# Performance work log

Measured on AMD Instinct MI355X. Metric: run time of the kernel, lower is better.

## Reference

```python
import jax, jax.numpy as jnp
import numpy as np

N = 8192
E = 262144
H = 64


def setup_inputs() -> dict:
    key = jax.random.key(0)
    ks = jax.random.split(key, 9)
    edge_index = jax.random.randint(ks[0], (2, E), 0, N, dtype=jnp.int64)
    edge_attr = jax.random.uniform(ks[1], (E,), dtype=jnp.float32)
    node_features = jax.random.normal(ks[2], (N, N), dtype=jnp.float32)
    # GCNConv weights (glorot-ish scale) and biases
    W1 = jax.random.normal(ks[3], (N, H), dtype=jnp.float32) / np.sqrt(N)
    b1 = jnp.zeros((H,), dtype=jnp.float32)
    W2 = jax.random.normal(ks[4], (H, H), dtype=jnp.float32) / np.sqrt(H)
    b2 = jnp.zeros((H,), dtype=jnp.float32)
    fcW = jax.random.normal(ks[5], (H, N), dtype=jnp.float32) / np.sqrt(H)
    fcb = jnp.zeros((N,), dtype=jnp.float32)
    return {"edge_index": edge_index, "edge_attr": edge_attr,
            "node_features": node_features,
            "W1": W1, "b1": b1, "W2": W2, "b2": b2,
            "fcW": fcW, "fcb": fcb}


def _gcn_conv(x, W, b, src, dst, ew, n_nodes):
    # PyG GCNConv with edge weights: x' = D^{-1/2} (A + I) D^{-1/2} (x W) + b
    # src/dst/ew already include self-loops (weight 1.0).
    x = x @ W                                        # [N, out]
    deg = jax.ops.segment_sum(ew, dst, num_segments=n_nodes)  # in-degree w/ loops
    dinv = jax.lax.rsqrt(deg)                        # deg >= 1 due to self loops
    norm = dinv[src] * ew * dinv[dst]                # [E+N]
    out = jax.ops.segment_sum(x[src] * norm[:, None], dst, num_segments=n_nodes)
    return out + b


def reference(edge_index, edge_attr, node_features, W1, b1, W2, b2, fcW, fcb):
    n_nodes = node_features.shape[0]
    loops = jnp.arange(n_nodes, dtype=edge_index.dtype)
    src = jnp.concatenate([edge_index[0], loops])
    dst = jnp.concatenate([edge_index[1], loops])
    ew = jnp.concatenate([edge_attr, jnp.ones((n_nodes,), edge_attr.dtype)])
    x = jax.nn.relu(_gcn_conv(node_features, W1, b1, src, dst, ew, n_nodes))
    x = jax.nn.relu(_gcn_conv(x, W2, b2, src, dst, ew, n_nodes))
    x = x @ fcW + fcb
    return jax.nn.softmax(x, axis=-1)
```

## Files before the change

kernel.cpp:

```cpp
#include <hip/hip_runtime.h>


#define NN 8192
#define NE 262144
#define HD 64
#define KCH 1024
#define NKC 8

typedef float f32x4 __attribute__((ext_vector_type(4)));
typedef short v8s   __attribute__((ext_vector_type(8)));
typedef unsigned short ushort_t;

__device__ __forceinline__ unsigned short bf16_rne(float f){
  union { float f; unsigned u; } v; v.f = f;
  unsigned r = v.u + 0x7fffu + ((v.u >> 16) & 1u);
  return (unsigned short)(r >> 16);
}
__device__ __forceinline__ float bf16_f32(unsigned short h){
  union { unsigned u; float f; } v; v.u = ((unsigned)h) << 16;
  return v.f;
}
__device__ __forceinline__ f32x4 mfma16(v8s a, v8s b, f32x4 c){
  return __builtin_amdgcn_mfma_f32_16x16x32_bf16(a, b, c, 0, 0, 0);
}

__device__ __forceinline__ void split_tr(float f, short& hi, short& lo){
  unsigned u = __float_as_uint(f);
  hi = (short)(u >> 16);
  float fh = __uint_as_float(u & 0xffff0000u);
  float d = f - fh;
  lo = (short)(__float_as_uint(d) >> 16);
}

__global__ void k_prep0(const float* __restrict__ W1, const float* __restrict__ fcW,
                        ushort_t* w1hi, ushort_t* w1lo, ushort_t* fcwp,
                        float* deg, int* cnt, int* wcnt, float* S){
  int idx = blockIdx.x*blockDim.x + threadIdx.x;
  if (idx < NN){ deg[idx]=1.0f; cnt[idx]=0; wcnt[idx]=0; S[idx]=0.0f; }
  {
    int kk = idx & 31, c = (idx>>5)&15, nt = (idx>>9)&3, kb = idx>>11;
    int k = kb*32 + kk, col = nt*16 + c;
    float w = W1[(size_t)k*HD + col];
    unsigned short hi = bf16_rne(w);
    w1hi[idx] = hi;
    w1lo[idx] = bf16_rne(w - bf16_f32(hi));
  }
  {
    int kk = idx & 31, c = (idx>>5)&15, cblk = (idx>>9)&511, kb = idx>>18;
    int k = kb*32 + kk, col = cblk*16 + c;
    fcwp[idx] = bf16_rne(fcW[(size_t)k*NN + col]);
  }
}

__global__ void k_deg_cnt(const int* ei, const float* ew, float* deg, int* cnt){
  int e = blockIdx.x*blockDim.x + threadIdx.x;
  if (e < NE){
    int d = ei[NE + e];
    atomicAdd(&deg[d], ew[e]);
    atomicAdd(&cnt[d], 1);
  }
}

__global__ void k_scan(const int* cnt, const float* deg, int* rowptr, float* dinv){
  __shared__ int part[256];
  int t = threadIdx.x;
  int loc[32]; int s = 0;
  #pragma unroll
  for (int j=0;j<32;++j){ loc[j] = cnt[t*32+j]; s += loc[j]; }
  part[t] = s; __syncthreads();
  for (int off=1; off<256; off<<=1){
    int v = (t >= off) ? part[t-off] : 0;
    __syncthreads();
    part[t] += v;
    __syncthreads();
  }
  int run = part[t] - s;
  #pragma unroll
  for (int j=0;j<32;++j){ rowptr[t*32+j] = run; run += loc[j]; }
  if (t == 255) rowptr[NN] = run;
  #pragma unroll
  for (int j=0;j<32;++j) dinv[t*32+j] = 1.0f / sqrtf(deg[t*32+j]);
}

__global__ void k_fill(const int* ei, const float* ew, const float* dinv,
                       const int* rowptr, int* wcnt, int* csr_src, float* csr_nrm){
  int e = blockIdx.x*blockDim.x + threadIdx.x;
  if (e < NE){
    int s = ei[e], d = ei[NE+e];
    int slot = rowptr[d] + atomicAdd(&wcnt[d], 1);
    csr_src[slot] = s;
    csr_nrm[slot] = dinv[s] * ew[e] * dinv[d];
  }
}

__global__ __launch_bounds__(256, 2) void k_gemm1(const float* __restrict__ X,
                                                  const ushort_t* __restrict__ w1hi,
                                                  const ushort_t* __restrict__ w1lo,
                                                  float* __restrict__ xw1p){
  int lane = threadIdx.x & 63, w = threadIdx.x >> 6;
  int r = lane & 15, seg = lane >> 4;
  int row0 = blockIdx.x*128 + w*32;
  int kb0 = blockIdx.y * KCH;
  const float* xr0 = X + (size_t)(row0 + r)      * NN + kb0 + seg*8;
  const float* xr1 = X + (size_t)(row0 + 16 + r) * NN + kb0 + seg*8;
  const ushort_t* bhp = w1hi + (size_t)(kb0 >> 5)*2048 + r*32 + seg*8;
  const ushort_t* blp = w1lo + (size_t)(kb0 >> 5)*2048 + r*32 + seg*8;

  f32x4 z = {0.f,0.f,0.f,0.f};
  f32x4 acc0[4] = {z,z,z,z};
  f32x4 acc1[4] = {z,z,z,z};

  f32x4 A00_0, A01_0, A10_0, A11_0;
  f32x4 A00_1, A01_1, A10_1, A11_1;
  v8s bh0[4], bl0[4], bh1[4], bl1[4];

  A00_0 = *(const f32x4*)(xr0);        A01_0 = *(const f32x4*)(xr0 + 4);
  A10_0 = *(const f32x4*)(xr1);        A11_0 = *(const f32x4*)(xr1 + 4);
  A00_1 = *(const f32x4*)(xr0 + 32);   A01_1 = *(const f32x4*)(xr0 + 36);
  A10_1 = *(const f32x4*)(xr1 + 32);   A11_1 = *(const f32x4*)(xr1 + 36);
  #pragma unroll
  for (int nt=0; nt<4; ++nt){
    bh0[nt] = *(const v8s*)(bhp + nt*512);
    bl0[nt] = *(const v8s*)(blp + nt*512);
    bh1[nt] = *(const v8s*)(bhp + 2048 + nt*512);
    bl1[nt] = *(const v8s*)(blp + 2048 + nt*512);
  }

  auto body = [&](int it, f32x4& A00, f32x4& A01, f32x4& A10, f32x4& A11,
                  v8s (&bh)[4], v8s (&bl)[4]){
    v8s ah0, al0, ah1, al1;
    #pragma unroll
    for (int j=0;j<4;++j){
      short h,l;
      split_tr(A00[j], h, l); ah0[j]   = h; al0[j]   = l;
      split_tr(A01[j], h, l); ah0[4+j] = h; al0[4+j] = l;
      split_tr(A10[j], h, l); ah1[j]   = h; al1[j]   = l;
      split_tr(A11[j], h, l); ah1[4+j] = h; al1[4+j] = l;
    }
    int itn = (it + 2) & 31;
    A00 = *(const f32x4*)(xr0 + itn*32);  A01 = *(const f32x4*)(xr0 + itn*32 + 4);
    A10 = *(const f32x4*)(xr1 + itn*32);  A11 = *(const f32x4*)(xr1 + itn*32 + 4);
    #pragma unroll
    for (int nt=0; nt<4; ++nt){
      acc0[nt] = mfma16(ah0, bh[nt], acc0[nt]);
      acc0[nt] = mfma16(ah0, bl[nt], acc0[nt]);
      acc0[nt] = mfma16(al0, bh[nt], acc0[nt]);
      acc1[nt] = mfma16(ah1, bh[nt], acc1[nt]);
      acc1[nt] = mfma16(ah1, bl[nt], acc1[nt]);
      acc1[nt] = mfma16(al1, bh[nt], acc1[nt]);
    }
    #pragma unroll
    for (int nt=0; nt<4; ++nt){
      bh[nt] = *(const v8s*)(bhp + (size_t)itn*2048 + nt*512);
      bl[nt] = *(const v8s*)(blp + (size_t)itn*2048 + nt*512);
    }
  };

  for (int j = 0; j < 16; ++j){
    body(2*j,     A00_0, A01_0, A10_0, A11_0, bh0, bl0);
    body(2*j + 1, A00_1, A01_1, A10_1, A11_1, bh1, bl1);
  }

  float* o = xw1p + (size_t)blockIdx.y*(NN*HD) + (size_t)row0*HD;
  #pragma unroll
  for (int nt=0; nt<4; ++nt)
    #pragma unroll
    for (int j=0;j<4;++j){
      o[(4*seg + j)*HD + nt*16 + r]        = acc0[nt][j];
      o[(16 + 4*seg + j)*HD + nt*16 + r]   = acc1[nt][j];
    }
}

__global__ __launch_bounds__(256) void k_red(const float* __restrict__ xw1p,
                                             float* __restrict__ xw1){
  int i = blockIdx.x*blockDim.x + threadIdx.x;
  f32x4 s = {0.f,0.f,0.f,0.f};
  #pragma unroll
  for (int c=0;c<NKC;++c){
    f32x4 v = *(const f32x4*)(xw1p + (size_t)c*NN*HD + (size_t)i*4);
    s[0]+=v[0]; s[1]+=v[1]; s[2]+=v[2]; s[3]+=v[3];
  }
  *(f32x4*)(xw1 + (size_t)i*4) = s;
}

__global__ __launch_bounds__(256) void k_agg1c(const float* __restrict__ xin,
                                               const float* __restrict__ b1,
                                               const float* __restrict__ W2,
                                               const float* __restrict__ dinv,
                                               const int* __restrict__ rowptr,
                                               const int* __restrict__ csr_src,
                                               const float* __restrict__ csr_nrm,
                                               float* __restrict__ x2w){
  __shared__ float W2s[64*64];
  __shared__ float rows[4][64];
  int lane = threadIdx.x & 63, w = threadIdx.x >> 6;
  for (int o = threadIdx.x; o < 64*64; o += 256) W2s[o] = W2[o];
  __syncthreads();

  int i = blockIdx.x*4 + w;
  float di = dinv[i];
  float acc = di*di * xin[(size_t)i*HD + lane];
  int e = rowptr[i], e1 = rowptr[i+1];
  for (; e + 1 < e1; e += 2){
    int s0 = csr_src[e], s1 = csr_src[e+1];
    float n0 = csr_nrm[e], n1 = csr_nrm[e+1];
    acc += n0 * xin[(size_t)s0*HD + lane];
    acc += n1 * xin[(size_t)s1*HD + lane];
  }
  if (e < e1) acc += csr_nrm[e] * xin[(size_t)csr_src[e]*HD + lane];
  float v = acc + b1[lane];
  rows[w][lane] = v > 0.f ? v : 0.f;
  __syncthreads();

  float acc2 = 0.f;
  #pragma unroll
  for (int k=0;k<64;++k) acc2 += rows[w][k] * W2s[k*64 + lane];
  x2w[(size_t)i*HD + lane] = acc2;
}

__global__ __launch_bounds__(256) void k_agg2(const float* __restrict__ xin,
                                              const float* __restrict__ b2,
                                              const float* __restrict__ dinv,
                                              const int* __restrict__ rowptr,
                                              const int* __restrict__ csr_src,
                                              const float* __restrict__ csr_nrm,
                                              ushort_t* __restrict__ x2b){
  int lane = threadIdx.x & 63, w = threadIdx.x >> 6;
  int i = blockIdx.x*4 + w;
  float di = dinv[i];
  float acc = di*di * xin[(size_t)i*HD + lane];
  int e = rowptr[i], e1 = rowptr[i+1];
  for (; e + 1 < e1; e += 2){
    int s0 = csr_src[e], s1 = csr_src[e+1];
    float n0 = csr_nrm[e], n1 = csr_nrm[e+1];
    acc += n0 * xin[(size_t)s0*HD + lane];
    acc += n1 * xin[(size_t)s1*HD + lane];
  }
  if (e < e1) acc += csr_nrm[e] * xin[(size_t)csr_src[e]*HD + lane];
  float v = acc + b2[lane];
  v = v > 0.f ? v : 0.f;
  x2b[(size_t)i*HD + lane] = bf16_rne(v);
}

__global__ __launch_bounds__(256) void k_rowsum(const ushort_t* __restrict__ x2b,
                                                const ushort_t* __restrict__ fcwp,
                                                const float* __restrict__ fcb,
                                                float* __restrict__ S){
  int lane = threadIdx.x & 63, w = threadIdx.x >> 6;
  int r = lane & 15, seg = lane >> 4;
  int row0 = blockIdx.x*128 + w*32;
  const ushort_t* xb = x2b + (size_t)(row0 + r)*HD + seg*8;
  v8s x00 = *(const v8s*)(xb);
  v8s x01 = *(const v8s*)(xb + 32);
  v8s x10 = *(const v8s*)(xb + 16*HD);
  v8s x11 = *(const v8s*)(xb + 16*HD + 32);
  float rp0 = 0.f, rp1 = 0.f;
  for (int cb=0; cb<4; ++cb){
    int colbase = blockIdx.y*256 + cb*64;
    f32x4 z = {0.f,0.f,0.f,0.f};
    f32x4 acc0[4] = {z,z,z,z}, acc1[4] = {z,z,z,z};
    #pragma unroll
    for (int nt=0; nt<4; ++nt){
      int cblk = (colbase >> 4) + nt;
      v8s bA = *(const v8s*)(fcwp + ((size_t)cblk*16 + r)*32 + seg*8);
      v8s bB = *(const v8s*)(fcwp + ((size_t)(512 + cblk)*16 + r)*32 + seg*8);
      acc0[nt] = mfma16(bA, x00, acc0[nt]);
      acc0[nt] = mfma16(bB, x01, acc0[nt]);
      acc1[nt] = mfma16(bA, x10, acc1[nt]);
      acc1[nt] = mfma16(bB, x11, acc1[nt]);
    }
    #pragma unroll
    for (int nt=0; nt<4; ++nt){
      int col = colbase + nt*16 + seg*4;
      f32x4 fb = *(const f32x4*)(fcb + col);
      #pragma unroll
      for (int j=0;j<4;++j){
        rp0 += __expf(acc0[nt][j] + fb[j]);
        rp1 += __expf(acc1[nt][j] + fb[j]);
      }
    }
  }
  rp0 += __shfl_xor(rp0, 16); rp0 += __shfl_xor(rp0, 32);
  rp1 += __shfl_xor(rp1, 16); rp1 += __shfl_xor(rp1, 32);
  if (lane < 16){
    atomicAdd(&S[row0 + lane],      rp0);
    atomicAdd(&S[row0 + 16 + lane], rp1);
  }
}

__global__ __launch_bounds__(256) void k_passB(const ushort_t* __restrict__ x2b,
                                               const ushort_t* __restrict__ fcwp,
                                               const float* __restrict__ fcb,
                                               const float* __restrict__ S,
                                               float* __restrict__ out){
  int lane = threadIdx.x & 63, w = threadIdx.x >> 6;
  int r = lane & 15, seg = lane >> 4;
  int row0 = blockIdx.x*128 + w*32;
  const ushort_t* xb = x2b + (size_t)(row0 + r)*HD + seg*8;
  v8s x00 = *(const v8s*)(xb);
  v8s x01 = *(const v8s*)(xb + 32);
  v8s x10 = *(const v8s*)(xb + 16*HD);
  v8s x11 = *(const v8s*)(xb + 16*HD + 32);
  float si0 = 1.0f / S[row0 + r];
  float si1 = 1.0f / S[row0 + 16 + r];
  float* o0 = out + (size_t)(row0 + r)*NN;
  float* o1 = out + (size_t)(row0 + 16 + r)*NN;
  for (int cb=0; cb<4; ++cb){
    int colbase = blockIdx.y*256 + cb*64;
    f32x4 z = {0.f,0.f,0.f,0.f};
    f32x4 acc0[4] = {z,z,z,z}, acc1[4] = {z,z,z,z};
    #pragma unroll
    for (int nt=0; nt<4; ++nt){
      int cblk = (colbase >> 4) + nt;
      v8s bA = *(const v8s*)(fcwp + ((size_t)cblk*16 + r)*32 + seg*8);
      v8s bB = *(const v8s*)(fcwp + ((size_t)(512 + cblk)*16 + r)*32 + seg*8);
      acc0[nt] = mfma16(bA, x00, acc0[nt]);
      acc0[nt] = mfma16(bB, x01, acc0[nt]);
      acc1[nt] = mfma16(bA, x10, acc1[nt]);
      acc1[nt] = mfma16(bB, x11, acc1[nt]);
    }
    #pragma unroll
    for (int nt=0; nt<4; ++nt){
      int col = colbase + nt*16 + seg*4;
      f32x4 fb = *(const f32x4*)(fcb + col);
      f32x4 v0, v1;
      #pragma unroll
      for (int j=0;j<4;++j){
        v0[j] = __expf(acc0[nt][j] + fb[j]) * si0;
        v1[j] = __expf(acc1[nt][j] + fb[j]) * si1;
      }
      *(f32x4*)(o0 + col) = v0;
      *(f32x4*)(o1 + col) = v1;
    }
  }
}

extern "C" void kernel_launch(void* const* d_in, const int* in_sizes, int n_in,
                              void* d_out, int out_size, void* d_ws, size_t ws_size,
                              hipStream_t stream){
  (void)in_sizes; (void)n_in; (void)out_size; (void)ws_size;
  const int*   ei  = (const int*)  d_in[0];
  const float* ew  = (const float*)d_in[1];
  const float* X   = (const float*)d_in[2];
  const float* W1  = (const float*)d_in[3];
  const float* b1  = (const float*)d_in[4];
  const float* W2  = (const float*)d_in[5];
  const float* b2  = (const float*)d_in[6];
  const float* fcW = (const float*)d_in[7];
  const float* fcb = (const float*)d_in[8];
  float* out = (float*)d_out;
  char*  ws  = (char*)d_ws;

  float*    deg     = (float*)   (ws + 0);
  float*    dinv    = (float*)   (ws + 32768);
  int*      cnt     = (int*)     (ws + 65536);
  int*      wcnt    = (int*)     (ws + 98304);
  int*      rowptr  = (int*)     (ws + 131072);
  int*      csr_src = (int*)     (ws + 167936);
  float*    csr_nrm = (float*)   (ws + 1216512);
  ushort_t* w1hi    = (ushort_t*)(ws + 2265088);
  ushort_t* w1lo    = (ushort_t*)(ws + 3313664);
  ushort_t* fcwp    = (ushort_t*)(ws + 4362240);
  float*    xw1p    = (float*)   (ws + 5410816);
  float*    xw1     = (float*)   (ws + 22188032);
  float*    x2w     = (float*)   (ws + 24285184);
  ushort_t* x2b     = (ushort_t*)(ws + 26382336);
  float*    S       = (float*)   (ws + 27430912);

  k_prep0   <<<2048, 256, 0, stream>>>(W1, fcW, w1hi, w1lo, fcwp, deg, cnt, wcnt, S);
  k_deg_cnt <<<1024, 256, 0, stream>>>(ei, ew, deg, cnt);
  k_scan    <<<1,    256, 0, stream>>>(cnt, deg, rowptr, dinv);
  k_fill    <<<1024, 256, 0, stream>>>(ei, ew, dinv, rowptr, wcnt, csr_src, csr_nrm);
  k_gemm1   <<<dim3(64, NKC), 256, 0, stream>>>(X, w1hi, w1lo, xw1p);
  k_red     <<<512,  256, 0, stream>>>(xw1p, xw1);
  k_agg1c   <<<2048, 256, 0, stream>>>(xw1, b1, W2, dinv, rowptr, csr_src, csr_nrm, x2w);
  k_agg2    <<<2048, 256, 0, stream>>>(x2w, b2, dinv, rowptr, csr_src, csr_nrm, x2b);
  k_rowsum  <<<dim3(64,32), 256, 0, stream>>>(x2b, fcwp, fcb, S);
  k_passB   <<<dim3(64,32), 256, 0, stream>>>(x2b, fcwp, fcb, S, out);
}
```

Measured before the change: 302.6 us.

## Stage X tiles in LDS via async global_load_lds with swizzled double buffering

The dense first GEMM now streams X through a double-buffered, XOR-swizzled shared-memory tile filled by direct global-to-LDS loads, instead of register-prefetching strided rows. Block size drops to 128 threads with twice as many blocks. The aim is coalesced, latency-hidden loads of the large 256MB X matrix, which dominates runtime. It adds a per-iteration __syncthreads, and the B fragments are no longer prefetched a step ahead.

```diff
diff --git a/kernel.cpp b/kernel.cpp
--- a/kernel.cpp
+++ b/kernel.cpp
@@ -23,13 +23,17 @@
 __device__ __forceinline__ f32x4 mfma16(v8s a, v8s b, f32x4 c){
   return __builtin_amdgcn_mfma_f32_16x16x32_bf16(a, b, c, 0, 0, 0);
 }
-
 __device__ __forceinline__ void split_tr(float f, short& hi, short& lo){
   unsigned u = __float_as_uint(f);
   hi = (short)(u >> 16);
   float fh = __uint_as_float(u & 0xffff0000u);
   float d = f - fh;
   lo = (short)(__float_as_uint(d) >> 16);
+}
+__device__ __forceinline__ void gload16(const void* g, void* l){
+  __builtin_amdgcn_global_load_lds(
+      (const __attribute__((address_space(1))) unsigned int*)g,
+      (__attribute__((address_space(3))) unsigned int*)l, 16, 0, 0);
 }
 
 __global__ void k_prep0(const float* __restrict__ W1, const float* __restrict__ fcW,
@@ -93,16 +97,20 @@
   }
 }
 
-__global__ __launch_bounds__(256, 2) void k_gemm1(const float* __restrict__ X,
+__global__ __launch_bounds__(128, 2) void k_gemm1(const float* __restrict__ X,
                                                   const ushort_t* __restrict__ w1hi,
                                                   const ushort_t* __restrict__ w1lo,
                                                   float* __restrict__ xw1p){
+  __shared__ char bufA[2][64*128];
   int lane = threadIdx.x & 63, w = threadIdx.x >> 6;
   int r = lane & 15, seg = lane >> 4;
-  int row0 = blockIdx.x*128 + w*32;
+  int row0 = blockIdx.x*64;
   int kb0 = blockIdx.y * KCH;
-  const float* xr0 = X + (size_t)(row0 + r)      * NN + kb0 + seg*8;
-  const float* xr1 = X + (size_t)(row0 + 16 + r) * NN + kb0 + seg*8;
+
+  int srow = lane >> 3;
+  int scolb = ((lane & 7)*16) ^ ((srow & 7) << 4);
+  const char* g0 = (const char*)(X + (size_t)(row0 + w*32 + srow)*NN + kb0) + scolb;
+  const size_t gRow8 = (size_t)8*NN*4;
   const ushort_t* bhp = w1hi + (size_t)(kb0 >> 5)*2048 + r*32 + seg*8;
   const ushort_t* blp = w1lo + (size_t)(kb0 >> 5)*2048 + r*32 + seg*8;
 
@@ -110,24 +118,36 @@
   f32x4 acc0[4] = {z,z,z,z};
   f32x4 acc1[4] = {z,z,z,z};
 
-  f32x4 A00_0, A01_0, A10_0, A11_0;
-  f32x4 A00_1, A01_1, A10_1, A11_1;
-  v8s bh0[4], bl0[4], bh1[4], bl1[4];
-
-  A00_0 = *(const f32x4*)(xr0);        A01_0 = *(const f32x4*)(xr0 + 4);
-  A10_0 = *(const f32x4*)(xr1);        A11_0 = *(const f32x4*)(xr1 + 4);
-  A00_1 = *(const f32x4*)(xr0 + 32);   A01_1 = *(const f32x4*)(xr0 + 36);
-  A10_1 = *(const f32x4*)(xr1 + 32);   A11_1 = *(const f32x4*)(xr1 + 36);
-  #pragma unroll
-  for (int nt=0; nt<4; ++nt){
-    bh0[nt] = *(const v8s*)(bhp + nt*512);
-    bl0[nt] = *(const v8s*)(blp + nt*512);
-    bh1[nt] = *(const v8s*)(bhp + 2048 + nt*512);
-    bl1[nt] = *(const v8s*)(blp + 2048 + nt*512);
-  }
-
-  auto body = [&](int it, f32x4& A00, f32x4& A01, f32x4& A10, f32x4& A11,
-                  v8s (&bh)[4], v8s (&bl)[4]){
+  int swz = (r & 7) << 4;
+  int a0b = (w*32 + r)*128;
+  int a1b = (w*32 + 16 + r)*128;
+  int c0 = (seg*32) ^ swz;
+  int c1 = (seg*32 + 16) ^ swz;
+
+  #pragma unroll
+  for (int i=0;i<4;++i)
+    gload16(g0 + i*gRow8, &bufA[0][(w*32 + i*8)*128]);
+
+  const int NT = KCH/32;
+  for (int t = 0; t < NT; ++t){
+    __syncthreads();
+    int cur = t & 1;
+    if (t + 1 < NT){
+      #pragma unroll
+      for (int i=0;i<4;++i)
+        gload16(g0 + i*gRow8 + (size_t)(t+1)*128, &bufA[cur^1][(w*32 + i*8)*128]);
+    }
+    v8s bh[4], bl[4];
+    #pragma unroll
+    for (int nt=0; nt<4; ++nt){
+      bh[nt] = *(const v8s*)(bhp + (size_t)t*2048 + nt*512);
+      bl[nt] = *(const v8s*)(blp + (size_t)t*2048 + nt*512);
+    }
+    const char* base = bufA[cur];
+    f32x4 A00 = *(const f32x4*)(base + a0b + c0);
+    f32x4 A01 = *(const f32x4*)(base + a0b + c1);
+    f32x4 A10 = *(const f32x4*)(base + a1b + c0);
+    f32x4 A11 = *(const f32x4*)(base + a1b + c1);
     v8s ah0, al0, ah1, al1;
     #pragma unroll
     for (int j=0;j<4;++j){
@@ -137,9 +157,6 @@
       split_tr(A10[j], h, l); ah1[j]   = h; al1[j]   = l;
       split_tr(A11[j], h, l); ah1[4+j] = h; al1[4+j] = l;
     }
-    int itn = (it + 2) & 31;
-    A00 = *(const f32x4*)(xr0 + itn*32);  A01 = *(const f32x4*)(xr0 + itn*32 + 4);
-    A10 = *(const f32x4*)(xr1 + itn*32);  A11 = *(const f32x4*)(xr1 + itn*32 + 4);
     #pragma unroll
     for (int nt=0; nt<4; ++nt){
       acc0[nt] = mfma16(ah0, bh[nt], acc0[nt]);
@@ -149,19 +166,9 @@
       acc1[nt] = mfma16(ah1, bl[nt], acc1[nt]);
       acc1[nt] = mfma16(al1, bh[nt], acc1[nt]);
     }
-    #pragma unroll
-    for (int nt=0; nt<4; ++nt){
-      bh[nt] = *(const v8s*)(bhp + (size_t)itn*2048 + nt*512);
-      bl[nt] = *(const v8s*)(blp + (size_t)itn*2048 + nt*512);
-    }
-  };
-
-  for (int j = 0; j < 16; ++j){
-    body(2*j,     A00_0, A01_0, A10_0, A11_0, bh0, bl0);
-    body(2*j + 1, A00_1, A01_1, A10_1, A11_1, bh1, bl1);
-  }
-
-  float* o = xw1p + (size_t)blockIdx.y*(NN*HD) + (size_t)row0*HD;
+  }
+
+  float* o = xw1p + (size_t)blockIdx.y*(NN*HD) + (size_t)(row0 + w*32)*HD;
   #pragma unroll
   for (int nt=0; nt<4; ++nt)
     #pragma unroll
@@ -371,7 +378,7 @@
   k_deg_cnt <<<1024, 256, 0, stream>>>(ei, ew, deg, cnt);
   k_scan    <<<1,    256, 0, stream>>>(cnt, deg, rowptr, dinv);
   k_fill    <<<1024, 256, 0, stream>>>(ei, ew, dinv, rowptr, wcnt, csr_src, csr_nrm);
-  k_gemm1   <<<dim3(64, NKC), 256, 0, stream>>>(X, w1hi, w1lo, xw1p);
+  k_gemm1   <<<dim3(128, NKC), 128, 0, stream>>>(X, w1hi, w1lo, xw1p);
   k_red     <<<512,  256, 0, stream>>>(xw1p, xw1);
   k_agg1c   <<<2048, 256, 0, stream>>>(xw1, b1, W2, dinv, rowptr, csr_src, csr_nrm, x2w);
   k_agg2    <<<2048, 256, 0, stream>>>(x2w, b2, dinv, rowptr, csr_src, csr_nrm, x2b);
```

After: 293.4 us. 1.03x faster.
